# Kernel optimization log

Measured on AMD Instinct MI355X. Metric: run time of the kernel, lower is better.

## Reference

```python
import jax, jax.numpy as jnp
import numpy as np

ITERS = 3
EPS = 1e-6


def setup_inputs() -> dict:
    key = jax.random.key(0)
    k1, k2 = jax.random.split(key, 2)
    a = jax.random.normal(k1, (64, 1152, 1, 1, 1, 1), dtype=jnp.float32)
    v = jax.random.normal(k2, (64, 1152, 32, 4, 4, 1), dtype=jnp.float32)
    logits = jnp.ones((1, 1152, 32, 1, 1, 1), dtype=jnp.float32)
    return {"a": a, "v": v, "logits": logits}


def _squash(s):
    # s: (batch, 1, B, P, P, 1); norm over dim 2 (matches torch code, dim=2)
    norm_sq = jnp.sum(s * s, axis=2, keepdims=True)
    return jnp.sqrt(norm_sq + EPS) / (1.0 + norm_sq) * s


def reference(a, v, logits):
    # a: (batch, A, 1, 1, 1, 1) -- unused (overwritten in original forward)
    # v: (batch, A, B, P, P, 1); logits: (1, A, B, 1, 1, 1)
    batch = v.shape[0]
    b = jnp.broadcast_to(logits, (batch,) + logits.shape[1:])
    p = None
    for i in range(ITERS):
        c = jax.nn.softmax(b, axis=2)                    # route over B
        s = jnp.sum(c * v, axis=1, keepdims=True)        # (batch,1,B,P,P,1)
        p = _squash(s)
        if i < ITERS - 1:
            # agreement: sum over pose dims -> (batch, A, B, 1, 1, 1)
            b = b + jnp.sum(p * v, axis=(-3, -2, -1), keepdims=True)
    p = jnp.squeeze(p, axis=1)                           # (batch, B, P, P, 1)
    a_out = jnp.linalg.norm(p, ord=2, axis=2)            # (batch, B, P, 1)
    return (a_out, p)
```

## Files before the change

kernel.cpp:

```cpp
#include <hip/hip_runtime.h>
#include <math.h>

#define BATCH 64
#define ADIM  1152
#define BDIM  32
#define POSE  16
#define SLICE (BDIM * POSE)
#define CHUNKS 18
#define A_PER_CHUNK (ADIM / CHUNKS)
#define EPSQ 1e-6f

__global__ __launch_bounds__(256) void route_pass(
    const float* __restrict__ v,
    const float* __restrict__ logits,
    const float* __restrict__ p_buf,
    float* __restrict__ s_out,
    int iter)
{
    const int bt    = blockIdx.x / CHUNKS;
    const int chunk = blockIdx.x % CHUNKS;
    const int t     = threadIdx.x;
    const int bc    = t & 31;
    const int a_sub = t >> 5;

    __shared__ float p_sh[2][SLICE];
    __shared__ float red[8 * SLICE];

    for (int j = 0; j < iter; ++j)
        for (int idx = t; idx < SLICE; idx += 256)
            p_sh[j][idx] = p_buf[(size_t)j * BATCH * SLICE + (size_t)bt * SLICE + idx];
    __syncthreads();

    float acc[POSE];
#pragma unroll
    for (int k = 0; k < POSE; ++k) acc[k] = 0.f;

    const int a0 = chunk * A_PER_CHUNK;
    for (int ai = 0; ai < A_PER_CHUNK / 8; ++ai) {
        const int a = a0 + ai * 8 + a_sub;
        const float4* vp4 = reinterpret_cast<const float4*>(
            v + ((size_t)bt * ADIM + a) * SLICE + bc * POSE);
        float vv[POSE];
#pragma unroll
        for (int q = 0; q < 4; ++q) {
            float4 f = vp4[q];
            vv[q * 4 + 0] = f.x; vv[q * 4 + 1] = f.y;
            vv[q * 4 + 2] = f.z; vv[q * 4 + 3] = f.w;
        }

        float bval = logits[a * BDIM + bc];
        for (int j = 0; j < iter; ++j) {
            float d = 0.f;
#pragma unroll
            for (int k = 0; k < POSE; ++k) d += p_sh[j][bc * POSE + k] * vv[k];
            bval += d;
        }

        float m = bval;
#pragma unroll
        for (int off = 16; off > 0; off >>= 1)
            m = fmaxf(m, __shfl_xor(m, off, 32));
        float e = __expf(bval - m);
        float ssum = e;
#pragma unroll
        for (int off = 16; off > 0; off >>= 1)
            ssum += __shfl_xor(ssum, off, 32);
        float c = e / ssum;

#pragma unroll
        for (int k = 0; k < POSE; ++k) acc[k] = fmaf(c, vv[k], acc[k]);
    }

#pragma unroll
    for (int k = 0; k < POSE; ++k) red[a_sub * SLICE + bc * POSE + k] = acc[k];
    __syncthreads();

    for (int idx = t; idx < SLICE; idx += 256) {
        float s = 0.f;
#pragma unroll
        for (int asb = 0; asb < 8; ++asb) s += red[asb * SLICE + idx];
        atomicAdd(&s_out[(size_t)bt * SLICE + idx], s);
    }
}

__global__ __launch_bounds__(512) void squash_kernel(
    const float* __restrict__ s_in,
    float* __restrict__ p_out,
    float* __restrict__ out,
    int last)
{
    const int bt = blockIdx.x;
    const int t = threadIdx.x;
    const int pose = t & 15;

    __shared__ float sq[512];
    __shared__ float ns[16];

    float sv = s_in[(size_t)bt * SLICE + t];
    sq[t] = sv * sv;
    __syncthreads();
    if (t < 16) {
        float a = 0.f;
        for (int b2 = 0; b2 < BDIM; ++b2) a += sq[b2 * POSE + t];
        ns[t] = a;
    }
    __syncthreads();
    float n = ns[pose];
    float pv = sqrtf(n + EPSQ) / (1.f + n) * sv;
    p_out[(size_t)bt * SLICE + t] = pv;

    if (last) {
        out[8192 + bt * SLICE + t] = pv;
        sq[t] = pv * pv;
        __syncthreads();
        if (t < 128) {
            int b2 = t >> 2, p2 = t & 3;
            float a = 0.f;
#pragma unroll
            for (int p1 = 0; p1 < 4; ++p1) a += sq[b2 * POSE + p1 * 4 + p2];
            out[bt * 128 + b2 * 4 + p2] = sqrtf(a);
        }
    }
}

extern "C" void kernel_launch(void* const* d_in, const int* in_sizes, int n_in,
                              void* d_out, int out_size, void* d_ws, size_t ws_size,
                              hipStream_t stream) {
    const float* v      = (const float*)d_in[1];
    const float* logits = (const float*)d_in[2];
    float* out = (float*)d_out;

    float* s_buf = (float*)d_ws;
    float* p_buf = s_buf + 3 * BATCH * SLICE;

    hipMemsetAsync(s_buf, 0, (size_t)3 * BATCH * SLICE * sizeof(float), stream);

    for (int it = 0; it < 3; ++it) {
        route_pass<<<dim3(BATCH * CHUNKS), dim3(256), 0, stream>>>(
            v, logits, p_buf, s_buf + (size_t)it * BATCH * SLICE, it);
        squash_kernel<<<dim3(BATCH), dim3(512), 0, stream>>>(
            s_buf + (size_t)it * BATCH * SLICE,
            p_buf + (size_t)it * BATCH * SLICE,
            out, it == 2 ? 1 : 0);
    }
}
```

Measured before the change: 279.0 us.

## Stage v tiles through swizzled LDS with register prefetch, keep p in registers

Changes the route pass to load each 8-row v tile with fully coalesced float4 loads into XOR-swizzled shared memory, prefetching the next tile into registers while the current one is consumed. The previous iteration's p vectors are held in registers instead of shared memory, and the chunk count drops to 16 with 72 A rows each and a min-blocks launch bound. The goal is better global-load coalescing and latency hiding on a memory-bound pass over v. In exchange it adds two barriers per step and raises register pressure.

New measurement: 355.4 us. 27.4% more time.

```diff
diff --git a/kernel.cpp b/kernel.cpp
--- a/kernel.cpp
+++ b/kernel.cpp
@@ -5,12 +5,13 @@
 #define ADIM  1152
 #define BDIM  32
 #define POSE  16
-#define SLICE (BDIM * POSE)
-#define CHUNKS 18
-#define A_PER_CHUNK (ADIM / CHUNKS)
+#define SLICE 512
+#define CHUNKS 16
+#define A_PER_CHUNK 72
+#define STEPS 9
 #define EPSQ 1e-6f
 
-__global__ __launch_bounds__(256) void route_pass(
+__global__ __launch_bounds__(256, 4) void route_pass(
     const float* __restrict__ v,
     const float* __restrict__ logits,
     const float* __restrict__ p_buf,
@@ -23,36 +24,73 @@
     const int bc    = t & 31;
     const int a_sub = t >> 5;
 
-    __shared__ float p_sh[2][SLICE];
-    __shared__ float red[8 * SLICE];
+    __shared__ __align__(16) float smem[8 * SLICE];
+    float4* tile = (float4*)smem;
 
-    for (int j = 0; j < iter; ++j)
-        for (int idx = t; idx < SLICE; idx += 256)
-            p_sh[j][idx] = p_buf[(size_t)j * BATCH * SLICE + (size_t)bt * SLICE + idx];
-    __syncthreads();
+    float p0[POSE], p1[POSE];
+    if (iter >= 1) {
+        const float4* pp = (const float4*)(p_buf + (size_t)bt * SLICE + bc * POSE);
+#pragma unroll
+        for (int q = 0; q < 4; ++q) {
+            float4 f = pp[q];
+            p0[4*q+0]=f.x; p0[4*q+1]=f.y; p0[4*q+2]=f.z; p0[4*q+3]=f.w;
+        }
+    }
+    if (iter >= 2) {
+        const float4* pp = (const float4*)(p_buf + (size_t)(BATCH + bt) * SLICE + bc * POSE);
+#pragma unroll
+        for (int q = 0; q < 4; ++q) {
+            float4 f = pp[q];
+            p1[4*q+0]=f.x; p1[4*q+1]=f.y; p1[4*q+2]=f.z; p1[4*q+3]=f.w;
+        }
+    }
 
     float acc[POSE];
 #pragma unroll
     for (int k = 0; k < POSE; ++k) acc[k] = 0.f;
 
     const int a0 = chunk * A_PER_CHUNK;
-    for (int ai = 0; ai < A_PER_CHUNK / 8; ++ai) {
-        const int a = a0 + ai * 8 + a_sub;
-        const float4* vp4 = reinterpret_cast<const float4*>(
-            v + ((size_t)bt * ADIM + a) * SLICE + bc * POSE);
+    const float4* gbase = (const float4*)(v + ((size_t)bt * ADIM + a0) * SLICE);
+
+    float4 r[4];
+#pragma unroll
+    for (int i = 0; i < 4; ++i) r[i] = gbase[t + 256 * i];
+
+    for (int step = 0; step < STEPS; ++step) {
+#pragma unroll
+        for (int i = 0; i < 4; ++i) {
+            int L   = t + 256 * i;
+            int row = L >> 7;
+            int col = L & 127;
+            tile[row * 128 + (col ^ ((col >> 2) & 7))] = r[i];
+        }
+        __syncthreads();
+
+        if (step + 1 < STEPS) {
+            const float4* gnext = gbase + (size_t)(step + 1) * 1024;
+#pragma unroll
+            for (int i = 0; i < 4; ++i) r[i] = gnext[t + 256 * i];
+        }
+
         float vv[POSE];
 #pragma unroll
         for (int q = 0; q < 4; ++q) {
-            float4 f = vp4[q];
-            vv[q * 4 + 0] = f.x; vv[q * 4 + 1] = f.y;
-            vv[q * 4 + 2] = f.z; vv[q * 4 + 3] = f.w;
+            float4 f = tile[a_sub * 128 + ((bc * 4 + q) ^ (bc & 7))];
+            vv[4*q+0]=f.x; vv[4*q+1]=f.y; vv[4*q+2]=f.z; vv[4*q+3]=f.w;
         }
 
+        const int a = a0 + step * 8 + a_sub;
         float bval = logits[a * BDIM + bc];
-        for (int j = 0; j < iter; ++j) {
+        if (iter >= 1) {
             float d = 0.f;
 #pragma unroll
-            for (int k = 0; k < POSE; ++k) d += p_sh[j][bc * POSE + k] * vv[k];
+            for (int k = 0; k < POSE; ++k) d = fmaf(p0[k], vv[k], d);
+            bval += d;
+        }
+        if (iter >= 2) {
+            float d = 0.f;
+#pragma unroll
+            for (int k = 0; k < POSE; ++k) d = fmaf(p1[k], vv[k], d);
             bval += d;
         }
 
@@ -69,8 +107,10 @@
 
 #pragma unroll
         for (int k = 0; k < POSE; ++k) acc[k] = fmaf(c, vv[k], acc[k]);
+        __syncthreads();
     }
 
+    float* red = smem;
 #pragma unroll
     for (int k = 0; k < POSE; ++k) red[a_sub * SLICE + bc * POSE + k] = acc[k];
     __syncthreads();
```
